# Kernel optimization log

Hardware: AMD Instinct MI355X
Metric: run time of the kernel (lower is better)

## Reference

```python
import jax, jax.numpy as jnp
import numpy as np

D_MODEL = 512
NUM_HEADS = 8


def setup_inputs() -> dict:
    key = jax.random.key(0)
    ks = jax.random.split(key, 6)
    B, T, D = 4, 2048, D_MODEL
    x = jax.random.normal(ks[0], (B, T, D), dtype=jnp.float32)
    periods = jax.random.randint(ks[1], (B, NUM_HEADS), 0, 48)
    # nn.MultiheadAttention parameters: packed qkv in-projection + out-projection
    in_proj_w = jax.random.normal(ks[2], (3 * D, D), dtype=jnp.float32) * 0.02
    in_proj_b = jax.random.normal(ks[3], (3 * D,), dtype=jnp.float32) * 0.02
    out_w = jax.random.normal(ks[4], (D, D), dtype=jnp.float32) * 0.02
    out_b = jax.random.normal(ks[5], (D,), dtype=jnp.float32) * 0.02
    return {"x": x, "periods": periods, "in_proj_w": in_proj_w,
            "in_proj_b": in_proj_b, "out_w": out_w, "out_b": out_b}


def reference(x, periods, in_proj_w, in_proj_b, out_w, out_b):
    B, T, D = x.shape
    H = periods.shape[1]          # one head per period (num_heads == top_k)
    hd = D // H
    # packed qkv projection (matches torch in_proj_weight layout)
    qkv = x @ in_proj_w.T + in_proj_b            # (B,T,3D)
    q, k, v = jnp.split(qkv, 3, axis=-1)
    def to_heads(t):
        return t.reshape(B, T, H, hd).transpose(0, 2, 1, 3)  # (B,H,T,hd)
    q, k, v = to_heads(q), to_heads(k), to_heads(v)
    scores = jnp.einsum('bhqd,bhkd->bhqk', q, k) / jnp.sqrt(jnp.asarray(hd, x.dtype))
    # periodic causal mask: allow j<=i with (i-j) % P == 0
    i = jnp.arange(T)[:, None]
    j = jnp.arange(T)[None, :]
    p = jnp.maximum(periods, 1)[:, :, None, None]            # (B,H,1,1)
    allow = (j <= i) & (((i - j) % p) == 0)                  # (B,H,T,T)
    scores = jnp.where(allow, scores, -jnp.inf)              # diagonal always allowed -> no all-masked rows
    attn = jax.nn.softmax(scores, axis=-1)
    out = jnp.einsum('bhqk,bhkd->bhqd', attn, v)             # (B,H,T,hd)
    out = out.transpose(0, 2, 1, 3).reshape(B, T, D)
    return out @ out_w.T + out_b
```

## Files before the change

kernel.cpp:

```cpp
#include <hip/hip_runtime.h>
#include <math.h>

#define D_MODEL 512
#define NHEAD   8
#define HD      64
#define T_SEQ   2048
#define BATCH   4
#define M_ROWS  (BATCH * T_SEQ)

typedef __attribute__((ext_vector_type(8))) short  short8;
typedef __attribute__((ext_vector_type(4))) float  floatx4;

__device__ __forceinline__ unsigned short f2bf(float f) {
    unsigned int u = __float_as_uint(f);
    unsigned int r = u + 0x7FFFu + ((u >> 16) & 1u);
    return (unsigned short)(r >> 16);
}

__device__ __forceinline__ float bf2f(unsigned short u) {
    return __uint_as_float((unsigned int)u << 16);
}

__device__ __forceinline__ int4 cvt8(float4 a, float4 b) {
    union { unsigned short u[8]; int4 v; } r;
    r.u[0] = f2bf(a.x); r.u[1] = f2bf(a.y); r.u[2] = f2bf(a.z); r.u[3] = f2bf(a.w);
    r.u[4] = f2bf(b.x); r.u[5] = f2bf(b.y); r.u[6] = f2bf(b.z); r.u[7] = f2bf(b.w);
    return r.v;
}

__device__ __forceinline__ void gload16(const void* g, void* l) {
    __builtin_amdgcn_global_load_lds(
        (const __attribute__((address_space(1))) void*)g,
        (__attribute__((address_space(3))) void*)l, 16, 0, 0);
}

__device__ __forceinline__ bool slot_decode(int t, int P, int& r, int& mt, int& Lr)
{
    const int q0 = T_SEQ / P, rem = T_SEQ % P;
    const int nt_hi = (q0 + 64) >> 6;
    const int nt_lo = (q0 + 63) >> 6;
    const int hi_total = rem * nt_hi;
    if (t < hi_total) {
        r = t / nt_hi; mt = t - r * nt_hi; Lr = q0 + 1;
    } else {
        t -= hi_total;
        if (t >= (P - rem) * nt_lo) return false;
        const int rr = t / nt_lo;
        r = rem + rr; mt = t - rr * nt_lo; Lr = q0;
    }
    return true;
}

#define XGROUPS  (M_ROWS * D_MODEL / 8)
#define W1GROUPS (3 * D_MODEL * D_MODEL / 8)
#define W2GROUPS (D_MODEL * D_MODEL / 8)
#define CVT_GROUPS (XGROUPS + W1GROUPS + W2GROUPS)

__global__ __launch_bounds__(256) void cvt_inputs(
    const float* __restrict__ x, const float* __restrict__ w1,
    const float* __restrict__ w2, unsigned short* __restrict__ xo,
    unsigned short* __restrict__ w1o, unsigned short* __restrict__ w2o)
{
    int i = blockIdx.x * 256 + threadIdx.x;
    const float* src; unsigned short* dst;
    if (i < XGROUPS)                  { src = x;  dst = xo;  }
    else if (i < XGROUPS + W1GROUPS)  { src = w1; dst = w1o; i -= XGROUPS; }
    else                              { src = w2; dst = w2o; i -= XGROUPS + W1GROUPS; }
    const float4* p = (const float4*)(src + (size_t)i * 8);
    float4 a = p[0], b = p[1];
    *(int4*)(dst + (size_t)i * 8) = cvt8(a, b);
}

__global__ __launch_bounds__(256) void qkv_gemm_mfma(
    const unsigned short* __restrict__ X,
    const unsigned short* __restrict__ W,
    const float* __restrict__ bias,
    unsigned short* __restrict__ qo, unsigned short* __restrict__ ko,
    unsigned short* __restrict__ vo)
{
    __shared__ unsigned short smem[128 * 128];
    unsigned short* const As = smem;
    unsigned short* const Bs = smem + 128 * 64;

    const int bid  = blockIdx.x;
    const int xcd  = bid & 7;
    const int chk_ = bid >> 3;
    const int row0 = (((chk_ / 12) << 3) + xcd) << 7;
    const int col0 = (chk_ % 12) << 7;

    const int tid  = threadIdx.x;
    const int wave = tid >> 6, lane = tid & 63;
    const int quad = lane >> 4, l15 = lane & 15;
    const int wm   = wave >> 1, wn = wave & 1;
    const int lr8  = lane >> 3;
    const int sc   = lane & 7;

    floatx4 acc[4][4] = {};

    for (int k0 = 0; k0 < D_MODEL; k0 += 64) {
#pragma unroll
        for (int i = 0; i < 4; ++i) {
            const int rb  = (wave << 5) + (i << 3);
            const int r   = rb + lr8;
            const int csw = sc ^ (r & 7);
            gload16(X + (size_t)(row0 + r) * D_MODEL + k0 + (csw << 3),
                    As + (rb << 6));
            gload16(W + (size_t)(col0 + r) * D_MODEL + k0 + (csw << 3),
                    Bs + (rb << 6));
        }
        __syncthreads();

#pragma unroll
        for (int ks = 0; ks < 2; ++ks) {
            short8 af[4], bfr[4];
            const int ch = (ks << 2) + quad;
#pragma unroll
            for (int mt = 0; mt < 4; ++mt) {
                const int row = (wm << 6) + (mt << 4) + l15;
                af[mt] = *(const short8*)(As + (row << 6) + ((ch ^ (row & 7)) << 3));
            }
#pragma unroll
            for (int nt = 0; nt < 4; ++nt) {
                const int col = (wn << 6) + (nt << 4) + l15;
                bfr[nt] = *(const short8*)(Bs + (col << 6) + ((ch ^ (col & 7)) << 3));
            }
#pragma unroll
            for (int mt = 0; mt < 4; ++mt)
#pragma unroll
                for (int nt = 0; nt < 4; ++nt)
                    acc[mt][nt] = __builtin_amdgcn_mfma_f32_16x16x32_bf16(
                        af[mt], bfr[nt], acc[mt][nt], 0, 0, 0);
        }
        __syncthreads();
    }

#pragma unroll
    for (int nt = 0; nt < 4; ++nt) {
        const int ncol = (wn << 6) + (nt << 4) + l15;
        const float bn = bias[col0 + ncol];
#pragma unroll
        for (int mt = 0; mt < 4; ++mt)
#pragma unroll
            for (int reg = 0; reg < 4; ++reg) {
                const int mrow = (wm << 6) + (mt << 4) + (quad << 2) + reg;
                smem[(mrow << 7) + ncol] = f2bf(acc[mt][nt][reg] + bn);
            }
    }
    __syncthreads();
    {
        const int c16  = lane & 15;
        const int rsub = lane >> 4;
        const int n0   = col0 + (c16 << 3);
        const int part = n0 >> 9;
        unsigned short* dst = (part == 0) ? qo : ((part == 1) ? ko : vo);
        const int head = (n0 & 511) >> 6, d0 = n0 & 63;
#pragma unroll
        for (int p = 0; p < 8; ++p) {
            const int ml = (wave << 5) + (p << 2) + rsub;
            const int m  = row0 + ml;
            const int b = m >> 11, t = m & 2047;
            int4 val = *(const int4*)(smem + (ml << 7) + (c16 << 3));
            *(int4*)(dst + ((((size_t)b << 3) + head) * T_SEQ + t) * HD + d0) = val;
        }
    }
}

__global__ __launch_bounds__(256) void attn_rc_mfma(
    const unsigned short* __restrict__ q, const unsigned short* __restrict__ k,
    const unsigned short* __restrict__ v, const int* __restrict__ periods,
    unsigned short* __restrict__ o,
    unsigned short* __restrict__ Opart, float* __restrict__ Mpart,
    float* __restrict__ Lpart)
{
    __shared__ unsigned short Ks[2][64 * 64];
    __shared__ unsigned short Vt[2][64 * 64];
    __shared__ unsigned short Ps[64 * 64];

    const int bh = blockIdx.y;
    int P = periods[bh]; if (P < 1) P = 1;
    const int t_orig = blockIdx.x;
    const int c = blockIdx.z;
    int r, mt, Lr;
    if (!slot_decode(t_orig, P, r, mt, Lr)) return;
    if ((c << 3) > mt) return;
    const int nch  = (mt >> 3) + 1;
    const int kt0  = c << 3;
    const int kend = (kt0 + 7 < mt) ? (kt0 + 7) : mt;
    const int m0 = mt << 6;

    const int tid  = threadIdx.x;
    const int wave = tid >> 6, lane = tid & 63;
    const int quad = lane >> 4, l15 = lane & 15;
    const int srow = tid >> 2;
    const int vkp  = tid & 31, vhg = tid >> 5;

    const unsigned short* hq = q + (size_t)bh * T_SEQ * HD;
    const unsigned short* hk = k + (size_t)bh * T_SEQ * HD;
    const unsigned short* hv = v + (size_t)bh * T_SEQ * HD;

    const short8 vone = {16256, 16256, 16256, 16256,
                         16256, 16256, 16256, 16256};

    {
        int m = m0 + srow; if (m > Lr - 1) m = Lr - 1;
        const unsigned short* src = hq + (size_t)(r + m * P) * HD;
#pragma unroll
        for (int rep = 0; rep < 2; ++rep) {
            const int cc = ((tid & 3) << 1) + rep;
            int4 a = *(const int4*)(src + (cc << 3));
            *(int4*)(Ps + (srow << 6) + ((cc ^ (srow & 7)) << 3)) = a;
        }
    }
    {
        const int km0 = kt0 << 6;
        int mk = km0 + srow; if (mk > Lr - 1) mk = Lr - 1;
        const unsigned short* ksrc = hk + (size_t)(r + mk * P) * HD;
#pragma unroll
        for (int rep = 0; rep < 2; ++rep) {
            const int cc = ((tid & 3) << 1) + rep;
            int4 a = *(const int4*)(ksrc + (cc << 3));
            *(int4*)(Ks[0] + (srow << 6) + ((cc ^ (srow & 7)) << 3)) = a;
        }
        int mv0 = km0 + (vkp << 1);     if (mv0 > Lr - 1) mv0 = Lr - 1;
        int mv1 = km0 + (vkp << 1) + 1; if (mv1 > Lr - 1) mv1 = Lr - 1;
        int4 va = *(const int4*)(hv + (size_t)(r + mv0 * P) * HD + (vhg << 3));
        int4 vb = *(const int4*)(hv + (size_t)(r + mv1 * P) * HD + (vhg << 3));
        const unsigned short* pa = (const unsigned short*)&va;
        const unsigned short* pb = (const unsigned short*)&vb;
#pragma unroll
        for (int j = 0; j < 8; ++j) {
            const int hd_ = (vhg << 3) + j;
            const unsigned int pk =
                (unsigned int)pa[j] | ((unsigned int)pb[j] << 16);
            *(unsigned int*)((char*)Vt[0] + (hd_ << 7) +
                             ((((vkp >> 2) ^ (hd_ & 7)) << 4)) +
                             ((vkp & 3) << 2)) = pk;
        }
    }
    __syncthreads();
    short8 qf[2];
#pragma unroll
    for (int ks = 0; ks < 2; ++ks) {
        const int row = (wave << 4) + l15;
        qf[ks] = *(const short8*)(Ps + (row << 6) +
                                  ((((ks << 2) + quad) ^ (row & 7)) << 3));
    }

    floatx4 Oa[4] = {};
    float m_i[4] = {-1e30f, -1e30f, -1e30f, -1e30f};
    float l_i[4] = {0.f, 0.f, 0.f, 0.f};

    for (int kt = kt0; kt <= kend; ++kt) {
        const int buf = (kt - kt0) & 1;
        const bool havenext = kt < kend;

        int4 ka[2], va, vb;
        if (havenext) {
            const int km0 = (kt + 1) << 6;
            int mk = km0 + srow; if (mk > Lr - 1) mk = Lr - 1;
            const unsigned short* ksrc = hk + (size_t)(r + mk * P) * HD;
#pragma unroll
            for (int rep = 0; rep < 2; ++rep)
                ka[rep] = *(const int4*)(ksrc + ((((tid & 3) << 1) + rep) << 3));
            int mv0 = km0 + (vkp << 1);     if (mv0 > Lr - 1) mv0 = Lr - 1;
            int mv1 = km0 + (vkp << 1) + 1; if (mv1 > Lr - 1) mv1 = Lr - 1;
            va = *(const int4*)(hv + (size_t)(r + mv0 * P) * HD + (vhg << 3));
            vb = *(const int4*)(hv + (size_t)(r + mv1 * P) * HD + (vhg << 3));
        }

        floatx4 sacc[4] = {};
#pragma unroll
        for (int nt = 0; nt < 4; ++nt) {
            const int row = (nt << 4) + l15;
#pragma unroll
            for (int ks = 0; ks < 2; ++ks) {
                short8 kf = *(const short8*)(Ks[buf] + (row << 6) +
                                             ((((ks << 2) + quad) ^ (row & 7)) << 3));
                sacc[nt] = __builtin_amdgcn_mfma_f32_16x16x32_bf16(
                    qf[ks], kf, sacc[nt], 0, 0, 0);
            }
        }

        const bool diag = (kt == mt);
        float s[4][4];
        float tm = -1e30f;
#pragma unroll
        for (int nt = 0; nt < 4; ++nt)
#pragma unroll
            for (int reg = 0; reg < 4; ++reg) {
                float sv = sacc[nt][reg] * 0.125f;
                if (diag) {
                    const int sq = (wave << 4) + (quad << 2) + reg;
                    if (((nt << 4) + l15) > sq) sv = -1e30f;
                }
                s[nt][reg] = sv;
                tm = fmaxf(tm, sv);
            }
        tm = fmaxf(tm, __shfl_xor(tm, 1));
        tm = fmaxf(tm, __shfl_xor(tm, 2));
        tm = fmaxf(tm, __shfl_xor(tm, 4));
        tm = fmaxf(tm, __shfl_xor(tm, 8));
        tm = fmaxf(tm, __shfl_xor(tm, 16));
        tm = fmaxf(tm, __shfl_xor(tm, 32));

        float sc[4];
#pragma unroll
        for (int reg = 0; reg < 4; ++reg) {
            const float nm = fmaxf(m_i[reg], tm);
            sc[reg] = __expf(m_i[reg] - nm);
            m_i[reg] = nm;
        }

#pragma unroll
        for (int reg = 0; reg < 4; ++reg) {
            const int row = (wave << 4) + (quad << 2) + reg;
#pragma unroll
            for (int nt = 0; nt < 4; ++nt) {
                const int col = (nt << 4) + l15;
                *((unsigned short*)((char*)Ps + (row << 7) +
                                    (((col >> 3) ^ (row & 7)) << 4) +
                                    ((col & 7) << 1))) =
                    f2bf(__expf(s[nt][reg] - m_i[reg]));
            }
        }

        short8 pf[2];
#pragma unroll
        for (int ks = 0; ks < 2; ++ks) {
            const int row = (wave << 4) + l15;
            pf[ks] = *(const short8*)(Ps + (row << 6) +
                                      ((((ks << 2) + quad) ^ (row & 7)) << 3));
        }
        floatx4 ls = {};
        ls = __builtin_amdgcn_mfma_f32_16x16x32_bf16(pf[0], vone, ls, 0, 0, 0);
        ls = __builtin_amdgcn_mfma_f32_16x16x32_bf16(pf[1], vone, ls, 0, 0, 0);
#pragma unroll
        for (int reg = 0; reg < 4; ++reg)
            l_i[reg] = l_i[reg] * sc[reg] + ls[reg];

#pragma unroll
        for (int nt = 0; nt < 4; ++nt)
#pragma unroll
            for (int reg = 0; reg < 4; ++reg)
                Oa[nt][reg] *= sc[reg];
#pragma unroll
        for (int nt = 0; nt < 4; ++nt) {
            const int row = (nt << 4) + l15;
#pragma unroll
            for (int ks = 0; ks < 2; ++ks) {
                short8 vf = *(const short8*)(Vt[buf] + (row << 6) +
                                             ((((ks << 2) + quad) ^ (row & 7)) << 3));
                Oa[nt] = __builtin_amdgcn_mfma_f32_16x16x32_bf16(
                    pf[ks], vf, Oa[nt], 0, 0, 0);
            }
        }

        if (havenext) {
#pragma unroll
            for (int rep = 0; rep < 2; ++rep) {
                const int cc = ((tid & 3) << 1) + rep;
                *(int4*)(Ks[buf ^ 1] + (srow << 6) + ((cc ^ (srow & 7)) << 3)) = ka[rep];
            }
            const unsigned short* pa = (const unsigned short*)&va;
            const unsigned short* pb = (const unsigned short*)&vb;
#pragma unroll
            for (int j = 0; j < 8; ++j) {
                const int hd_ = (vhg << 3) + j;
                const unsigned int pk =
                    (unsigned int)pa[j] | ((unsigned int)pb[j] << 16);
                *(unsigned int*)((char*)Vt[buf ^ 1] + (hd_ << 7) +
                                 ((((vkp >> 2) ^ (hd_ & 7)) << 4)) +
                                 ((vkp & 3) << 2)) = pk;
            }
        }
        __syncthreads();
    }

    if (nch == 1) {
#pragma unroll
        for (int reg = 0; reg < 4; ++reg) {
            const float invl = 1.f / l_i[reg];
            const int row = (wave << 4) + (quad << 2) + reg;
#pragma unroll
            for (int nt = 0; nt < 4; ++nt)
                Ks[0][(row << 6) + (nt << 4) + l15] = f2bf(Oa[nt][reg] * invl);
        }
        const int lrow = lane >> 2;
        const int chk  = (lane & 3) << 1;
        const int ml   = (wave << 4) + lrow;
        const int m    = m0 + ml;
        if (m < Lr) {
            const size_t base = ((size_t)bh * T_SEQ + (r + m * P)) * HD;
            int4 w0 = *(const int4*)(Ks[0] + (ml << 6) + (chk << 3));
            int4 w1 = *(const int4*)(Ks[0] + (ml << 6) + ((chk + 1) << 3));
            *(int4*)(o + base + (chk << 3))       = w0;
            *(int4*)(o + base + ((chk + 1) << 3)) = w1;
        }
    } else {
        const size_t slot = ((size_t)((bh << 6) + t_orig) << 2) + c;
#pragma unroll
        for (int reg = 0; reg < 4; ++reg) {
            const int row = (wave << 4) + (quad << 2) + reg;
#pragma unroll
            for (int nt = 0; nt < 4; ++nt)
                Ks[0][(row << 6) + (nt << 4) + l15] = f2bf(Oa[nt][reg]);
            if (l15 == 0) {
                Mpart[slot * 64 + row] = m_i[reg];
                Lpart[slot * 64 + row] = l_i[reg];
            }
        }
        const int lrow = lane >> 2;
        const int chk  = (lane & 3) << 1;
        const int ml   = (wave << 4) + lrow;
        unsigned short* dst = Opart + slot * 4096 + (ml << 6);
        *(int4*)(dst + (chk << 3))       = *(const int4*)(Ks[0] + (ml << 6) + (chk << 3));
        *(int4*)(dst + ((chk + 1) << 3)) = *(const int4*)(Ks[0] + (ml << 6) + ((chk + 1) << 3));
    }
}

__global__ __launch_bounds__(256) void reduce_rc(
    const int* __restrict__ periods,
    const unsigned short* __restrict__ Opart, const float* __restrict__ Mpart,
    const float* __restrict__ Lpart, unsigned short* __restrict__ o)
{
    const int bh = blockIdx.y;
    int P = periods[bh]; if (P < 1) P = 1;
    const int t = blockIdx.x;
    int r, mt, Lr;
    if (!slot_decode(t, P, r, mt, Lr)) return;
    const int nch = (mt >> 3) + 1;
    if (nch < 2) return;

    const int tid = threadIdx.x;
    const int row = tid >> 2;
    const int cg  = (tid & 3) << 4;
    const int m   = (mt << 6) + row;
    if (m >= Lr) return;

    const size_t slot0 = (size_t)((bh << 6) + t) << 2;

    float mv[4], lv[4];
    float mm = -1e30f;
    for (int cc = 0; cc < nch; ++cc) {
        mv[cc] = Mpart[(slot0 + cc) * 64 + row];
        lv[cc] = Lpart[(slot0 + cc) * 64 + row];
        mm = fmaxf(mm, mv[cc]);
    }
    float lsum = 0.f, a[4];
    for (int cc = 0; cc < nch; ++cc) {
        a[cc] = __expf(mv[cc] - mm);
        lsum += a[cc] * lv[cc];
    }
    const float inv = 1.f / lsum;

    float ov[16] = {};
    for (int cc = 0; cc < nch; ++cc) {
        const unsigned short* p = Opart + (slot0 + cc) * 4096 + (row << 6) + cg;
        const float ac = a[cc];
#pragma unroll
        for (int j = 0; j < 16; ++j) ov[j] += ac * bf2f(p[j]);
    }
    unsigned short outv[16];
#pragma unroll
    for (int j = 0; j < 16; ++j) outv[j] = f2bf(ov[j] * inv);

    unsigned short* dst = o + ((size_t)bh * T_SEQ + (r + m * P)) * HD + cg;
    *(int4*)dst       = *(const int4*)&outv[0];
    *(int4*)(dst + 8) = *(const int4*)&outv[8];
}

__global__ __launch_bounds__(256) void out_gemm_mfma(
    const unsigned short* __restrict__ A,
    const unsigned short* __restrict__ W,
    const float* __restrict__ bias,
    float* __restrict__ out)
{
    __shared__ unsigned short As[128 * 64];
    __shared__ unsigned short Bs[128 * 64];

    const int tid  = threadIdx.x;
    const int wave = tid >> 6, lane = tid & 63;
    const int quad = lane >> 4, l15 = lane & 15;
    const int wm   = wave >> 1, wn = wave & 1;
    const int row0 = blockIdx.x * 128;
    const int col0 = blockIdx.y * 128;
    const int lr8  = lane >> 3;
    const int sc   = lane & 7;

    floatx4 acc[4][4] = {};

    for (int k0 = 0; k0 < D_MODEL; k0 += 64) {
        const int h = k0 >> 6;
#pragma unroll
        for (int i = 0; i < 4; ++i) {
            const int rb  = (wave << 5) + (i << 3);
            const int r   = rb + lr8;
            const int csw = sc ^ (r & 7);
            const int rg = row0 + r;
            const int b = rg >> 11, t = rg & 2047;
            gload16(A + ((((size_t)b << 3) + h) * T_SEQ + t) * HD + (csw << 3),
                    As + (rb << 6));
            gload16(W + (size_t)(col0 + r) * D_MODEL + k0 + (csw << 3),
                    Bs + (rb << 6));
        }
        __syncthreads();

#pragma unroll
        for (int ks = 0; ks < 2; ++ks) {
            short8 af[4], bfr[4];
            const int ch = (ks << 2) + quad;
#pragma unroll
            for (int mt = 0; mt < 4; ++mt) {
                const int row = (wm << 6) + (mt << 4) + l15;
                af[mt] = *(const short8*)(As + (row << 6) + ((ch ^ (row & 7)) << 3));
            }
#pragma unroll
            for (int nt = 0; nt < 4; ++nt) {
                const int col = (wn << 6) + (nt << 4) + l15;
                bfr[nt] = *(const short8*)(Bs + (col << 6) + ((ch ^ (col & 7)) << 3));
            }
#pragma unroll
            for (int mt = 0; mt < 4; ++mt)
#pragma unroll
                for (int nt = 0; nt < 4; ++nt)
                    acc[mt][nt] = __builtin_amdgcn_mfma_f32_16x16x32_bf16(
                        af[mt], bfr[nt], acc[mt][nt], 0, 0, 0);
        }
        __syncthreads();
    }

#pragma unroll
    for (int nt = 0; nt < 4; ++nt) {
        const int n = col0 + (wn << 6) + (nt << 4) + l15;
        const float bn = bias[n];
#pragma unroll
        for (int mt = 0; mt < 4; ++mt) {
#pragma unroll
            for (int reg = 0; reg < 4; ++reg) {
                const int m = row0 + (wm << 6) + (mt << 4) + (quad << 2) + reg;
                out[(size_t)m * D_MODEL + n] = acc[mt][nt][reg] + bn;
            }
        }
    }
}

extern "C" void kernel_launch(void* const* d_in, const int* in_sizes, int n_in,
                              void* d_out, int out_size, void* d_ws, size_t ws_size,
                              hipStream_t stream)
{
    const float* x        = (const float*)d_in[0];
    const int*   periods  = (const int*)  d_in[1];
    const float* in_w     = (const float*)d_in[2];
    const float* in_b     = (const float*)d_in[3];
    const float* out_w    = (const float*)d_in[4];
    const float* out_b    = (const float*)d_in[5];
    float*       out      = (float*)d_out;

    const size_t TENS = (size_t)BATCH * NHEAD * T_SEQ * HD;
    unsigned short* qb    = (unsigned short*)d_ws;
    unsigned short* kb    = qb + TENS;
    unsigned short* vb    = kb + TENS;
    unsigned short* aob   = vb + TENS;
    unsigned short* Opart = aob + TENS;
    float*          Mpart = (float*)(Opart + (size_t)8192 * 4096);
    float*          Lpart = Mpart + (size_t)8192 * 64;
    unsigned short* Xb    = (unsigned short*)(Lpart + (size_t)8192 * 64);
    unsigned short* W1b   = Xb + (size_t)M_ROWS * D_MODEL;
    unsigned short* W2b   = W1b + (size_t)3 * D_MODEL * D_MODEL;

    cvt_inputs<<<CVT_GROUPS / 256, 256, 0, stream>>>(x, in_w, out_w, Xb, W1b, W2b);

    qkv_gemm_mfma<<<(M_ROWS / 128) * ((3 * D_MODEL) / 128), 256, 0, stream>>>(
        Xb, W1b, in_b, qb, kb, vb);

    dim3 g2(64, BATCH * NHEAD, 4);
    attn_rc_mfma<<<g2, 256, 0, stream>>>(qb, kb, vb, periods, aob,
                                         Opart, Mpart, Lpart);
    reduce_rc<<<dim3(64, BATCH * NHEAD), 256, 0, stream>>>(
        periods, Opart, Mpart, Lpart, aob);

    dim3 g3(M_ROWS / 128, D_MODEL / 128);
    out_gemm_mfma<<<g3, 256, 0, stream>>>(aob, W2b, out_b, out);
}
```

Baseline: 151.6 us.

## Use exp2 softmax with lazy rescaling, MFMA priority hints, smaller out-GEMM tiles

```diff
diff --git a/kernel.cpp b/kernel.cpp
--- a/kernel.cpp
+++ b/kernel.cpp
@@ -19,6 +19,12 @@
 
 __device__ __forceinline__ float bf2f(unsigned short u) {
     return __uint_as_float((unsigned int)u << 16);
+}
+
+__device__ __forceinline__ float exp2_raw(float x) {
+    float r;
+    asm("v_exp_f32 %0, %1" : "=v"(r) : "v"(x));
+    return r;
 }
 
 __device__ __forceinline__ int4 cvt8(float4 a, float4 b) {
@@ -165,6 +171,8 @@
     }
 }
 
+#define SCALE2 0.18033688011112042f
+
 __global__ __launch_bounds__(256) void attn_rc_mfma(
     const unsigned short* __restrict__ q, const unsigned short* __restrict__ k,
     const unsigned short* __restrict__ v, const int* __restrict__ periods,
@@ -269,6 +277,7 @@
         }
 
         floatx4 sacc[4] = {};
+        __builtin_amdgcn_s_setprio(1);
 #pragma unroll
         for (int nt = 0; nt < 4; ++nt) {
             const int row = (nt << 4) + l15;
@@ -280,6 +289,7 @@
                     qf[ks], kf, sacc[nt], 0, 0, 0);
             }
         }
+        __builtin_amdgcn_s_setprio(0);
 
         const bool diag = (kt == mt);
         float s[4][4];
@@ -288,7 +298,7 @@
         for (int nt = 0; nt < 4; ++nt)
 #pragma unroll
             for (int reg = 0; reg < 4; ++reg) {
-                float sv = sacc[nt][reg] * 0.125f;
+                float sv = sacc[nt][reg] * SCALE2;
                 if (diag) {
                     const int sq = (wave << 4) + (quad << 2) + reg;
                     if (((nt << 4) + l15) > sq) sv = -1e30f;
@@ -303,12 +313,19 @@
         tm = fmaxf(tm, __shfl_xor(tm, 16));
         tm = fmaxf(tm, __shfl_xor(tm, 32));
 
-        float sc[4];
-#pragma unroll
-        for (int reg = 0; reg < 4; ++reg) {
-            const float nm = fmaxf(m_i[reg], tm);
-            sc[reg] = __expf(m_i[reg] - nm);
-            m_i[reg] = nm;
+        bool grow = (tm > m_i[0] + 8.f) | (tm > m_i[1] + 8.f) |
+                    (tm > m_i[2] + 8.f) | (tm > m_i[3] + 8.f);
+        if (__any(grow)) {
+#pragma unroll
+            for (int reg = 0; reg < 4; ++reg) {
+                const float nm = fmaxf(m_i[reg], tm);
+                const float sc = exp2_raw(m_i[reg] - nm);
+                m_i[reg] = nm;
+                l_i[reg] *= sc;
+#pragma unroll
+                for (int nt = 0; nt < 4; ++nt)
+                    Oa[nt][reg] *= sc;
+            }
         }
 
 #pragma unroll
@@ -320,7 +337,7 @@
                 *((unsigned short*)((char*)Ps + (row << 7) +
                                     (((col >> 3) ^ (row & 7)) << 4) +
                                     ((col & 7) << 1))) =
-                    f2bf(__expf(s[nt][reg] - m_i[reg]));
+                    f2bf(exp2_raw(s[nt][reg] - m_i[reg]));
             }
         }
 
@@ -336,13 +353,9 @@
         ls = __builtin_amdgcn_mfma_f32_16x16x32_bf16(pf[1], vone, ls, 0, 0, 0);
 #pragma unroll
         for (int reg = 0; reg < 4; ++reg)
-            l_i[reg] = l_i[reg] * sc[reg] + ls[reg];
-
-#pragma unroll
-        for (int nt = 0; nt < 4; ++nt)
-#pragma unroll
-            for (int reg = 0; reg < 4; ++reg)
-                Oa[nt][reg] *= sc[reg];
+            l_i[reg] += ls[reg];
+
+        __builtin_amdgcn_s_setprio(1);
 #pragma unroll
         for (int nt = 0; nt < 4; ++nt) {
             const int row = (nt << 4) + l15;
@@ -354,6 +367,7 @@
                     pf[ks], vf, Oa[nt], 0, 0, 0);
             }
         }
+        __builtin_amdgcn_s_setprio(0);
 
         if (havenext) {
 #pragma unroll
@@ -448,7 +462,7 @@
     }
     float lsum = 0.f, a[4];
     for (int cc = 0; cc < nch; ++cc) {
-        a[cc] = __expf(mv[cc] - mm);
+        a[cc] = exp2_raw(mv[cc] - mm);
         lsum += a[cc] * lv[cc];
     }
     const float inv = 1.f / lsum;
@@ -475,43 +489,49 @@
     const float* __restrict__ bias,
     float* __restrict__ out)
 {
-    __shared__ unsigned short As[128 * 64];
+    __shared__ unsigned short As[64 * 64];
     __shared__ unsigned short Bs[128 * 64];
 
     const int tid  = threadIdx.x;
     const int wave = tid >> 6, lane = tid & 63;
     const int quad = lane >> 4, l15 = lane & 15;
     const int wm   = wave >> 1, wn = wave & 1;
-    const int row0 = blockIdx.x * 128;
+    const int row0 = blockIdx.x * 64;
     const int col0 = blockIdx.y * 128;
     const int lr8  = lane >> 3;
     const int sc   = lane & 7;
 
-    floatx4 acc[4][4] = {};
+    floatx4 acc[2][4] = {};
 
     for (int k0 = 0; k0 < D_MODEL; k0 += 64) {
         const int h = k0 >> 6;
 #pragma unroll
         for (int i = 0; i < 4; ++i) {
             const int rb  = (wave << 5) + (i << 3);
+            const int r   = rb + lr8;
+            const int csw = sc ^ (r & 7);
+            gload16(W + (size_t)(col0 + r) * D_MODEL + k0 + (csw << 3),
+                    Bs + (rb << 6));
+        }
+#pragma unroll
+        for (int i = 0; i < 2; ++i) {
+            const int rb  = (wave << 4) + (i << 3);
             const int r   = rb + lr8;
             const int csw = sc ^ (r & 7);
             const int rg = row0 + r;
             const int b = rg >> 11, t = rg & 2047;
             gload16(A + ((((size_t)b << 3) + h) * T_SEQ + t) * HD + (csw << 3),
                     As + (rb << 6));
-            gload16(W + (size_t)(col0 + r) * D_MODEL + k0 + (csw << 3),
-                    Bs + (rb << 6));
         }
         __syncthreads();
 
 #pragma unroll
         for (int ks = 0; ks < 2; ++ks) {
-            short8 af[4], bfr[4];
+            short8 af[2], bfr[4];
             const int ch = (ks << 2) + quad;
 #pragma unroll
-            for (int mt = 0; mt < 4; ++mt) {
-                const int row = (wm << 6) + (mt << 4) + l15;
+            for (int mt = 0; mt < 2; ++mt) {
+                const int row = (wm << 5) + (mt << 4) + l15;
                 af[mt] = *(const short8*)(As + (row << 6) + ((ch ^ (row & 7)) << 3));
             }
 #pragma unroll
@@ -520,7 +540,7 @@
                 bfr[nt] = *(const short8*)(Bs + (col << 6) + ((ch ^ (col & 7)) << 3));
             }
 #pragma unroll
-            for (int mt = 0; mt < 4; ++mt)
+            for (int mt = 0; mt < 2; ++mt)
 #pragma unroll
                 for (int nt = 0; nt < 4; ++nt)
                     acc[mt][nt] = __builtin_amdgcn_mfma_f32_16x16x32_bf16(
@@ -534,10 +554,10 @@
         const int n = col0 + (wn << 6) + (nt << 4) + l15;
         const float bn = bias[n];
 #pragma unroll
-        for (int mt = 0; mt < 4; ++mt) {
+        for (int mt = 0; mt < 2; ++mt) {
 #pragma unroll
             for (int reg = 0; reg < 4; ++reg) {
-                const int m = row0 + (wm << 6) + (mt << 4) + (quad << 2) + reg;
+                const int m = row0 + (wm << 5) + (mt << 4) + (quad << 2) + reg;
                 out[(size_t)m * D_MODEL + n] = acc[mt][nt][reg] + bn;
             }
         }
@@ -579,6 +599,6 @@
     reduce_rc<<<dim3(64, BATCH * NHEAD), 256, 0, stream>>>(
         periods, Opart, Mpart, Lpart, aob);
 
-    dim3 g3(M_ROWS / 128, D_MODEL / 128);
+    dim3 g3(M_ROWS / 64, D_MODEL / 128);
     out_gemm_mfma<<<g3, 256, 0, stream>>>(aob, W2b, out_b, out);
 }
```

Result: no change. 149.6 us (-1.3%).
